# Performance work log

Hardware: AMD Instinct MI355X
Metric: run time of the kernel (lower is better)

## Reference

```python
import jax, jax.numpy as jnp
import numpy as np

B, S, D, V, T, NS, NG = 16, 512, 400, 32000, 8, 30, 3


def setup_inputs() -> dict:
    key = jax.random.key(0)
    ks = jax.random.split(key, 14)
    w = 1.0 / np.sqrt(D)
    return {
        "encoded_hidden": jax.random.normal(ks[0], (1, B, D), jnp.float32) * 0.1,
        "encoded_outputs": jax.random.normal(ks[1], (B, S, D), jnp.float32) * 0.1,
        "story": jax.random.randint(ks[2], (B, S), 0, V),
        "trg_batches": jax.random.randint(ks[3], (B, NS, T), 0, V),
        "shared_emb": jax.random.normal(ks[4], (V, D), jnp.float32) * 0.1,
        "slot_emb": jax.random.normal(ks[5], (1, D), jnp.float32) * 0.1,
        "w_ih": jax.random.normal(ks[6], (3 * D, D), jnp.float32) * w,
        "w_hh": jax.random.normal(ks[7], (3 * D, D), jnp.float32) * w,
        "b_ih": jax.random.normal(ks[8], (3 * D,), jnp.float32) * w,
        "b_hh": jax.random.normal(ks[9], (3 * D,), jnp.float32) * w,
        "w_ratio_w": jax.random.normal(ks[10], (1, 3 * D), jnp.float32) * w,
        "w_ratio_b": jax.random.normal(ks[11], (1,), jnp.float32) * w,
        "w_gate_w": jax.random.normal(ks[12], (NG, D), jnp.float32) * w,
        "w_gate_b": jax.random.normal(ks[13], (NG,), jnp.float32) * w,
        "batch_size": B,
        "max_resp_len": T,
    }


def reference(encoded_hidden, encoded_outputs, story, trg_batches, shared_emb,
              slot_emb, w_ih, w_hh, b_ih, b_hh, w_ratio_w, w_ratio_b,
              w_gate_w, w_gate_b, batch_size, max_resp_len):
    # Original torch code returns inside the slot loop -> only slot 0 is decoded.
    # h0 is re-used as GRU initial state at EVERY step (no carried hidden), and
    # teacher forcing makes each step's input known, so all T steps vectorize.
    h0 = encoded_hidden[0]                         # (B, D)
    Bq, Tq = batch_size, max_resp_len
    Vq = shared_emb.shape[0]

    # decoder inputs: step 0 = slot embedding, steps 1..T-1 = emb(trg[:,0,i-1])
    x0 = jnp.broadcast_to(slot_emb, h0.shape)      # (B, D)
    xt = shared_emb[trg_batches[:, 0, : Tq - 1]]   # (B, T-1, D)
    X = jnp.concatenate([x0[:, None, :], xt], axis=1)  # (B, T, D)

    # GRU cell (torch gate order r, z, n), h0 broadcast over steps
    gi = X @ w_ih.T + b_ih                         # (B, T, 3D)
    gh = h0 @ w_hh.T + b_hh                        # (B, 3D)
    i_r, i_z, i_n = jnp.split(gi, 3, axis=-1)
    h_r, h_z, h_n = jnp.split(gh, 3, axis=-1)
    r = jax.nn.sigmoid(i_r + h_r[:, None, :])
    z = jax.nn.sigmoid(i_z + h_z[:, None, :])
    n = jnp.tanh(i_n + r * h_n[:, None, :])
    h = (1.0 - z) * n + z * h0[:, None, :]         # (B, T, D) decoder_state == hidden

    # attention over history (no length masking: all lens == S)
    scores = jnp.einsum('btd,bsd->bts', h, encoded_outputs)   # (B, T, S)
    probs = jax.nn.softmax(scores, axis=-1)
    # FAITHFUL to original bug: context uses raw scores, not probs
    context = jnp.einsum('bts,bsd->btd', scores, encoded_outputs)

    gate0 = context[:, 0, :] @ w_gate_w.T + w_gate_b          # (B, NG), step i==0

    p_vocab = jax.nn.softmax(h @ shared_emb.T, axis=-1)       # (B, T, V)
    p_gen = jax.nn.sigmoid(
        jnp.concatenate([h, context, X], axis=-1) @ w_ratio_w.T + w_ratio_b
    )                                                         # (B, T, 1)

    # pointer distribution: scatter_add probs onto vocab ids of the story
    p_ctx = jnp.zeros((Bq, Tq, Vq), p_vocab.dtype).at[
        jnp.arange(Bq)[:, None, None],
        jnp.arange(Tq)[None, :, None],
        story[:, None, :],
    ].add(probs)

    p_final = p_gen * p_vocab + (1.0 - p_gen) * p_ctx         # (B, T, V)

    ptr_outputs = jnp.zeros((NS, Bq, Tq, Vq), p_final.dtype).at[0].set(p_final)
    gate_outputs = jnp.zeros((NS, Bq, NG), gate0.dtype).at[0].set(gate0)
    return ptr_outputs, gate_outputs
```

## Files before the change

kernel.cpp:

```cpp
#include <hip/hip_runtime.h>

#define Bq 16
#define Sq 512
#define Dq 400
#define Vq 32000
#define Tq 8
#define NSq 30
#define NGq 3
#define BTq (Bq*Tq)
#define SLICE 4096000
#define PTR_TOTAL (30ull*SLICE)
#define GATE_TOTAL (NSq*Bq*NGq)

#define ZTOT 29696000ull
#define ZPER 16384
#define GZB 256
#define AZB 384
#define LZB 1173

#define NCOMPUTE 250
#define GCOMPUTE 64

#define FBLK 8
#define FCH (Vq/FBLK)

__device__ inline float sigmoidf_(float x) { return 1.0f / (1.0f + __expf(-x)); }

__device__ inline unsigned bf16rne(float x) {
    unsigned u = __float_as_uint(x);
    return (u + 0x7FFFu + ((u >> 16) & 1u)) >> 16;
}

__device__ inline float blockReduceSum(float v, float* red) {
    int tid = threadIdx.x;
    #pragma unroll
    for (int o = 32; o > 0; o >>= 1) v += __shfl_down(v, o, 64);
    if ((tid & 63) == 0) red[tid >> 6] = v;
    __syncthreads();
    if (tid == 0) {
        float s = red[0];
        int nw = blockDim.x >> 6;
        for (int i = 1; i < nw; i++) s += red[i];
        red[0] = s;
    }
    __syncthreads();
    float r = red[0];
    __syncthreads();
    return r;
}

__device__ inline float blockReduceMax(float v, float* red) {
    int tid = threadIdx.x;
    #pragma unroll
    for (int o = 32; o > 0; o >>= 1) v = fmaxf(v, __shfl_down(v, o, 64));
    if ((tid & 63) == 0) red[tid >> 6] = v;
    __syncthreads();
    if (tid == 0) {
        float s = red[0];
        int nw = blockDim.x >> 6;
        for (int i = 1; i < nw; i++) s = fmaxf(s, red[i]);
        red[0] = s;
    }
    __syncthreads();
    float r = red[0];
    __syncthreads();
    return r;
}

__global__ __launch_bounds__(256) void k_gates(const float* __restrict__ enc_hidden,
                                               const float* __restrict__ shared_emb,
                                               const float* __restrict__ slot_emb,
                                               const float* __restrict__ w_ih,
                                               const float* __restrict__ w_hh,
                                               const float* __restrict__ b_ih,
                                               const float* __restrict__ b_hh,
                                               const int* __restrict__ trg,
                                               float* __restrict__ gi, float* __restrict__ gh,
                                               float* __restrict__ out) {
    int tid = threadIdx.x;
    if (blockIdx.x >= GCOMPUTE) {
        int zb = blockIdx.x - GCOMPUTE;
        float4 z = make_float4(0.0f, 0.0f, 0.0f, 0.0f);
        float4* dst = (float4*)(out + (size_t)SLICE);
        size_t base = (size_t)zb * ZPER + tid;
        #pragma unroll
        for (int r = 0; r < ZPER / 256; ++r) {
            size_t idx = base + (size_t)r * 256;
            if (idx < ZTOT) dst[idx] = z;
        }
        return;
    }
    __shared__ float A[9][Dq];
    __shared__ int toks[8];
    int b = blockIdx.x >> 2, jt = blockIdx.x & 3;
    if (tid < 7) toks[tid + 1] = trg[b * (NSq * Tq) + tid];
    __syncthreads();
    for (int idx = tid; idx < 900; idx += 256) {
        int r = idx / 100, q = idx - r * 100;
        const float4* src;
        if (r == 8)      src = (const float4*)(enc_hidden + b * Dq);
        else if (r == 0) src = (const float4*)slot_emb;
        else             src = (const float4*)(shared_emb + (size_t)toks[r] * Dq);
        *(float4*)&A[r][4 * q] = src[q];
    }
    __syncthreads();
    for (int o = tid; o < 2700; o += 256) {
        int r = o / 300, jj = o - r * 300;
        int j = jt * 300 + jj;
        const float* w = (r == 8) ? w_hh : w_ih;
        const float4* w4 = (const float4*)(w + (size_t)j * Dq);
        const float4* a4 = (const float4*)&A[r][0];
        float acc = (r == 8) ? b_hh[j] : b_ih[j];
        #pragma unroll 4
        for (int q = 0; q < Dq / 4; ++q) {
            float4 wv = w4[q], av = a4[q];
            acc += av.x * wv.x + av.y * wv.y + av.z * wv.z + av.w * wv.w;
        }
        if (r == 8) gh[b * 1200 + j] = acc;
        else        gi[(b * 8 + r) * 1200 + j] = acc;
    }
}

__global__ __launch_bounds__(512) void k_attn(const float* __restrict__ gi,
                                              const float* __restrict__ gh,
                                              const float* __restrict__ enc_hidden,
                                              const float* __restrict__ shared_emb,
                                              const float* __restrict__ slot_emb,
                                              const int* __restrict__ trg,
                                              const float* __restrict__ enc_out,
                                              const int* __restrict__ story,
                                              const float* __restrict__ w_ratio_w,
                                              const float* __restrict__ w_ratio_b,
                                              const float* __restrict__ w_gate_w,
                                              const float* __restrict__ w_gate_b,
                                              float* __restrict__ probs, float* __restrict__ pgen,
                                              float* __restrict__ hT, float* __restrict__ out_gate,
                                              float* __restrict__ out) {
    int tid = threadIdx.x;
    if (blockIdx.x >= BTq) {
        int zb = GZB + (blockIdx.x - BTq);
        float4 z = make_float4(0.0f, 0.0f, 0.0f, 0.0f);
        float4* dst = (float4*)(out + (size_t)SLICE);
        size_t base = (size_t)zb * ZPER + tid;
        #pragma unroll
        for (int r = 0; r < ZPER / 512; ++r) {
            size_t idx = base + (size_t)r * 512;
            if (idx < ZTOT) dst[idx] = z;
        }
        return;
    }
    __shared__ float h_l[Dq], ctx_l[Dq], x_l[Dq], sc_l[Sq], red[8];
    int bt = blockIdx.x, b = bt >> 3, t = bt & 7;
    if (tid < Dq) {
        int d = tid;
        float x = (t == 0) ? slot_emb[d]
                           : shared_emb[(size_t)trg[b * (NSq * Tq) + (t - 1)] * Dq + d];
        float h0 = enc_hidden[b * Dq + d];
        const float* gib = gi + bt * 1200;
        const float* ghb = gh + b * 1200;
        float r_ = sigmoidf_(gib[d] + ghb[d]);
        float z  = sigmoidf_(gib[Dq + d] + ghb[Dq + d]);
        float n  = tanhf(gib[2 * Dq + d] + r_ * ghb[2 * Dq + d]);
        float h  = (1.0f - z) * n + z * h0;
        h_l[d] = h; x_l[d] = x;
        hT[d * BTq + bt] = h;
    }
    __syncthreads();
    {
        const float4* e4 = (const float4*)(enc_out + ((size_t)(b * Sq + tid)) * Dq);
        float acc = 0.0f;
        for (int q = 0; q < Dq / 4; ++q) {
            float4 p = e4[q];
            int k = 4 * q;
            acc += h_l[k]*p.x + h_l[k+1]*p.y + h_l[k+2]*p.z + h_l[k+3]*p.w;
        }
        sc_l[tid] = acc;
    }
    __syncthreads();
    float myv = sc_l[tid];
    float m = blockReduceMax(myv, red);
    float e = __expf(myv - m);
    float ssum = blockReduceSum(e, red);
    probs[bt * Sq + tid] = e / ssum;
    for (int d = tid; d < Dq; d += 512) {
        float acc = 0.0f;
        #pragma unroll 8
        for (int s = 0; s < Sq; ++s)
            acc += sc_l[s] * enc_out[((size_t)(b * Sq + s)) * Dq + d];
        ctx_l[d] = acc;
    }
    __syncthreads();
    {
        float part = 0.0f;
        for (int i = tid; i < 1200; i += 512) {
            float v = (i < Dq) ? h_l[i] : (i < 2 * Dq ? ctx_l[i - Dq] : x_l[i - 2 * Dq]);
            part += v * w_ratio_w[i];
        }
        float tot = blockReduceSum(part, red);
        if (tid == 0) pgen[bt] = sigmoidf_(tot + w_ratio_b[0]);
    }
    if (t == 0) {
        for (int g = 0; g < NGq; ++g) {
            float part = 0.0f;
            for (int d = tid; d < Dq; d += 512) part += ctx_l[d] * w_gate_w[g * Dq + d];
            float tot = blockReduceSum(part, red);
            if (tid == 0) out_gate[b * NGq + g] = tot + w_gate_b[g];
        }
    }
}

#define TVL 128
#define CKL 40
__global__ __launch_bounds__(256) void k_logits(const float* __restrict__ hT,
                                                const float* __restrict__ emb,
                                                unsigned short* __restrict__ logits,
                                                float* __restrict__ pmax,
                                                float* __restrict__ psum,
                                                float* __restrict__ out) {
    __shared__ float eT[CKL][132];
    __shared__ float hL[CKL][132];
    int bid = blockIdx.x;
    int tid = threadIdx.x;
    if (bid >= NCOMPUTE) {
        int zl = bid - NCOMPUTE;
        float4 z = make_float4(0.0f, 0.0f, 0.0f, 0.0f);
        if (zl < LZB) {
            int zb = GZB + AZB + zl;
            float4* dst = (float4*)(out + (size_t)SLICE);
            size_t base = (size_t)zb * ZPER + tid;
            #pragma unroll
            for (int r = 0; r < ZPER / 256; ++r) {
                size_t idx = base + (size_t)r * 256;
                if (idx < ZTOT) dst[idx] = z;
            }
        } else {
            float4* g = (float4*)(out + PTR_TOTAL + Bq * NGq);
            for (int i = tid; i < (GATE_TOTAL - Bq * NGq) / 4; i += 256) g[i] = z;
        }
        return;
    }
    int v0 = bid * TVL;
    int tx = tid & 15, ty = tid >> 4;
    float acc[8][8];
    #pragma unroll
    for (int j = 0; j < 8; ++j)
        #pragma unroll
        for (int i = 0; i < 8; ++i) acc[j][i] = 0.0f;

    for (int c = 0; c < Dq / CKL; ++c) {
        int k0 = c * CKL;
        const float4* hg = (const float4*)(hT + (size_t)k0 * BTq);
        #pragma unroll
        for (int r = 0; r < 5; ++r) {
            int idx = tid + 256 * r;
            int k = idx >> 5, c4 = idx & 31;
            float4 vd = hg[idx];
            *(float4*)&hL[k][4 * c4] = vd;
        }
        #pragma unroll
        for (int r = 0; r < 5; ++r) {
            int idx = tid + 256 * r;
            int v = idx / 10, q = idx - 10 * v;
            float4 vd = *(const float4*)(emb + (size_t)(v0 + v) * Dq + k0 + 4 * q);
            eT[4*q+0][v] = vd.x; eT[4*q+1][v] = vd.y; eT[4*q+2][v] = vd.z; eT[4*q+3][v] = vd.w;
        }
        __syncthreads();
        #pragma unroll 4
        for (int k = 0; k < CKL; ++k) {
            float4 h0 = *(const float4*)&hL[k][8 * ty];
            float4 h1 = *(const float4*)&hL[k][8 * ty + 4];
            float4 e0 = *(const float4*)&eT[k][8 * tx];
            float4 e1 = *(const float4*)&eT[k][8 * tx + 4];
            float hv[8] = {h0.x, h0.y, h0.z, h0.w, h1.x, h1.y, h1.z, h1.w};
            float ev[8] = {e0.x, e0.y, e0.z, e0.w, e1.x, e1.y, e1.z, e1.w};
            #pragma unroll
            for (int j = 0; j < 8; ++j)
                #pragma unroll
                for (int i = 0; i < 8; ++i)
                    acc[j][i] += hv[j] * ev[i];
        }
        __syncthreads();
    }
    #pragma unroll
    for (int j = 0; j < 8; ++j) {
        int bt = 8 * ty + j;
        unsigned bb[8];
        float r[8];
        float m = -1e30f;
        #pragma unroll
        for (int i = 0; i < 8; ++i) {
            bb[i] = bf16rne(acc[j][i]);
            r[i] = __uint_as_float(bb[i] << 16);
            m = fmaxf(m, r[i]);
        }
        #pragma unroll
        for (int o = 8; o >= 1; o >>= 1) m = fmaxf(m, __shfl_xor(m, o, 16));
        float es = 0.0f;
        #pragma unroll
        for (int i = 0; i < 8; ++i) es += __expf(r[i] - m);
        #pragma unroll
        for (int o = 8; o >= 1; o >>= 1) es += __shfl_xor(es, o, 16);
        if (tx == 0) {
            pmax[bid * BTq + bt] = m;
            psum[bid * BTq + bt] = es;
        }
        uint4 w = make_uint4(bb[0] | (bb[1] << 16), bb[2] | (bb[3] << 16),
                             bb[4] | (bb[5] << 16), bb[6] | (bb[7] << 16));
        *(uint4*)(logits + (size_t)bt * Vq + v0 + 8 * tx) = w;
    }
}

__global__ __launch_bounds__(256) void k_final(const unsigned short* __restrict__ logits,
                                               const float* __restrict__ probs,
                                               const int* __restrict__ story,
                                               const float* __restrict__ pgen,
                                               const float* __restrict__ pmax,
                                               const float* __restrict__ psum,
                                               float* __restrict__ out) {
    __shared__ float chunk[FCH];
    __shared__ float red[4];
    int bid = blockIdx.x, tid = threadIdx.x;
    int bt = bid >> 3, ch = bid & 7, b = bt >> 3;
    float pm = (tid < NCOMPUTE) ? pmax[tid * BTq + bt] : -1e30f;
    float m = blockReduceMax(pm, red);
    float part = (tid < NCOMPUTE) ? psum[tid * BTq + bt] * __expf(pm - m) : 0.0f;
    float s = blockReduceSum(part, red);
    float inv = 1.0f / s, pg = pgen[bt], cg = 1.0f - pg;
    int lo = ch * FCH;
    const uint4* l4 = (const uint4*)(logits + (size_t)bt * Vq + lo);
    for (int i = tid; i < FCH / 8; i += 256) {
        uint4 lv = l4[i];
        float f0 = __uint_as_float(lv.x << 16), f1 = __uint_as_float(lv.x & 0xFFFF0000u);
        float f2 = __uint_as_float(lv.y << 16), f3 = __uint_as_float(lv.y & 0xFFFF0000u);
        float f4 = __uint_as_float(lv.z << 16), f5 = __uint_as_float(lv.z & 0xFFFF0000u);
        float f6 = __uint_as_float(lv.w << 16), f7 = __uint_as_float(lv.w & 0xFFFF0000u);
        chunk[8 * i + 0] = pg * __expf(f0 - m) * inv;
        chunk[8 * i + 1] = pg * __expf(f1 - m) * inv;
        chunk[8 * i + 2] = pg * __expf(f2 - m) * inv;
        chunk[8 * i + 3] = pg * __expf(f3 - m) * inv;
        chunk[8 * i + 4] = pg * __expf(f4 - m) * inv;
        chunk[8 * i + 5] = pg * __expf(f5 - m) * inv;
        chunk[8 * i + 6] = pg * __expf(f6 - m) * inv;
        chunk[8 * i + 7] = pg * __expf(f7 - m) * inv;
    }
    __syncthreads();
    for (int ss = tid; ss < Sq; ss += 256) {
        int rel = story[b * Sq + ss] - lo;
        if (rel >= 0 && rel < FCH)
            atomicAdd(&chunk[rel], cg * probs[bt * Sq + ss]);
    }
    __syncthreads();
    float4* o4 = (float4*)(out + (size_t)bt * Vq + lo);
    const float4* c4 = (const float4*)chunk;
    for (int i = tid; i < FCH / 4; i += 256) o4[i] = c4[i];
}

extern "C" void kernel_launch(void* const* d_in, const int* in_sizes, int n_in,
                              void* d_out, int out_size, void* d_ws, size_t ws_size,
                              hipStream_t stream) {
    const float* enc_hidden = (const float*)d_in[0];
    const float* enc_out    = (const float*)d_in[1];
    const int*   story      = (const int*)d_in[2];
    const int*   trg        = (const int*)d_in[3];
    const float* shared_emb = (const float*)d_in[4];
    const float* slot_emb   = (const float*)d_in[5];
    const float* w_ih       = (const float*)d_in[6];
    const float* w_hh       = (const float*)d_in[7];
    const float* b_ih       = (const float*)d_in[8];
    const float* b_hh       = (const float*)d_in[9];
    const float* w_ratio_w  = (const float*)d_in[10];
    const float* w_ratio_b  = (const float*)d_in[11];
    const float* w_gate_w   = (const float*)d_in[12];
    const float* w_gate_b   = (const float*)d_in[13];

    float* out = (float*)d_out;

    float* ws = (float*)d_ws;
    unsigned short* logits_buf = (unsigned short*)ws;
    float* probs_buf  = ws + (size_t)SLICE;
    float* gi_buf     = ws + 2 * (size_t)SLICE;
    float* gh_buf     = gi_buf + 153600;
    float* hT_buf     = gh_buf + 19200;
    float* pgen_buf   = hT_buf + 51200;
    float* pmax_buf   = pgen_buf + 128;
    float* psum_buf   = pmax_buf + 32000;

    hipLaunchKernelGGL(k_gates, dim3(GCOMPUTE + GZB), dim3(256), 0, stream,
                       enc_hidden, shared_emb, slot_emb, w_ih, w_hh, b_ih, b_hh, trg,
                       gi_buf, gh_buf, out);
    hipLaunchKernelGGL(k_attn, dim3(BTq + AZB), dim3(512), 0, stream,
                       gi_buf, gh_buf, enc_hidden, shared_emb, slot_emb, trg,
                       enc_out, story, w_ratio_w, w_ratio_b, w_gate_w, w_gate_b,
                       probs_buf, pgen_buf, hT_buf, out + PTR_TOTAL, out);
    hipLaunchKernelGGL(k_logits, dim3(NCOMPUTE + LZB + 1), dim3(256), 0, stream,
                       hT_buf, shared_emb, logits_buf, pmax_buf, psum_buf, out);
    hipLaunchKernelGGL(k_final, dim3(BTq * FBLK), dim3(256), 0, stream,
                       logits_buf, probs_buf, story, pgen_buf, pmax_buf, psum_buf, out);
}
```

Baseline: 742.6 us.

## Fuse GRU gate matvecs into attention kernel and use nontemporal zero stores

Removes the separate k_gates launch and computes the GRU input and hidden gate projections inside each k_attn block, keeping the results in shared memory instead of a global workspace. Its zero-fill blocks are folded into k_attn and k_logits by retuning the block counts. The large zero-fill and final output writes now use nontemporal stores to avoid polluting the cache. In exchange, each of the 128 attention blocks recomputes the hidden-state projection redundantly and streams the full w_ih and w_hh matrices, adding per-block latency before attention starts.

```diff
diff --git a/kernel.cpp b/kernel.cpp
--- a/kernel.cpp
+++ b/kernel.cpp
@@ -14,15 +14,15 @@
 
 #define ZTOT 29696000ull
 #define ZPER 16384
-#define GZB 256
-#define AZB 384
+#define AZB 640
 #define LZB 1173
 
 #define NCOMPUTE 250
-#define GCOMPUTE 64
 
 #define FBLK 8
 #define FCH (Vq/FBLK)
+
+typedef float f4nt __attribute__((ext_vector_type(4)));
 
 __device__ inline float sigmoidf_(float x) { return 1.0f / (1.0f + __expf(-x)); }
 
@@ -67,65 +67,13 @@
     return r;
 }
 
-__global__ __launch_bounds__(256) void k_gates(const float* __restrict__ enc_hidden,
-                                               const float* __restrict__ shared_emb,
-                                               const float* __restrict__ slot_emb,
-                                               const float* __restrict__ w_ih,
-                                               const float* __restrict__ w_hh,
-                                               const float* __restrict__ b_ih,
-                                               const float* __restrict__ b_hh,
-                                               const int* __restrict__ trg,
-                                               float* __restrict__ gi, float* __restrict__ gh,
-                                               float* __restrict__ out) {
-    int tid = threadIdx.x;
-    if (blockIdx.x >= GCOMPUTE) {
-        int zb = blockIdx.x - GCOMPUTE;
-        float4 z = make_float4(0.0f, 0.0f, 0.0f, 0.0f);
-        float4* dst = (float4*)(out + (size_t)SLICE);
-        size_t base = (size_t)zb * ZPER + tid;
-        #pragma unroll
-        for (int r = 0; r < ZPER / 256; ++r) {
-            size_t idx = base + (size_t)r * 256;
-            if (idx < ZTOT) dst[idx] = z;
-        }
-        return;
-    }
-    __shared__ float A[9][Dq];
-    __shared__ int toks[8];
-    int b = blockIdx.x >> 2, jt = blockIdx.x & 3;
-    if (tid < 7) toks[tid + 1] = trg[b * (NSq * Tq) + tid];
-    __syncthreads();
-    for (int idx = tid; idx < 900; idx += 256) {
-        int r = idx / 100, q = idx - r * 100;
-        const float4* src;
-        if (r == 8)      src = (const float4*)(enc_hidden + b * Dq);
-        else if (r == 0) src = (const float4*)slot_emb;
-        else             src = (const float4*)(shared_emb + (size_t)toks[r] * Dq);
-        *(float4*)&A[r][4 * q] = src[q];
-    }
-    __syncthreads();
-    for (int o = tid; o < 2700; o += 256) {
-        int r = o / 300, jj = o - r * 300;
-        int j = jt * 300 + jj;
-        const float* w = (r == 8) ? w_hh : w_ih;
-        const float4* w4 = (const float4*)(w + (size_t)j * Dq);
-        const float4* a4 = (const float4*)&A[r][0];
-        float acc = (r == 8) ? b_hh[j] : b_ih[j];
-        #pragma unroll 4
-        for (int q = 0; q < Dq / 4; ++q) {
-            float4 wv = w4[q], av = a4[q];
-            acc += av.x * wv.x + av.y * wv.y + av.z * wv.z + av.w * wv.w;
-        }
-        if (r == 8) gh[b * 1200 + j] = acc;
-        else        gi[(b * 8 + r) * 1200 + j] = acc;
-    }
-}
-
-__global__ __launch_bounds__(512) void k_attn(const float* __restrict__ gi,
-                                              const float* __restrict__ gh,
-                                              const float* __restrict__ enc_hidden,
+__global__ __launch_bounds__(512) void k_attn(const float* __restrict__ enc_hidden,
                                               const float* __restrict__ shared_emb,
                                               const float* __restrict__ slot_emb,
+                                              const float* __restrict__ w_ih,
+                                              const float* __restrict__ w_hh,
+                                              const float* __restrict__ b_ih,
+                                              const float* __restrict__ b_hh,
                                               const int* __restrict__ trg,
                                               const float* __restrict__ enc_out,
                                               const int* __restrict__ story,
@@ -138,31 +86,53 @@
                                               float* __restrict__ out) {
     int tid = threadIdx.x;
     if (blockIdx.x >= BTq) {
-        int zb = GZB + (blockIdx.x - BTq);
-        float4 z = make_float4(0.0f, 0.0f, 0.0f, 0.0f);
-        float4* dst = (float4*)(out + (size_t)SLICE);
+        int zb = blockIdx.x - BTq;
+        f4nt z = (f4nt)(0.0f);
+        f4nt* dst = (f4nt*)(out + (size_t)SLICE);
         size_t base = (size_t)zb * ZPER + tid;
         #pragma unroll
         for (int r = 0; r < ZPER / 512; ++r) {
             size_t idx = base + (size_t)r * 512;
-            if (idx < ZTOT) dst[idx] = z;
+            if (idx < ZTOT) __builtin_nontemporal_store(z, &dst[idx]);
         }
         return;
     }
-    __shared__ float h_l[Dq], ctx_l[Dq], x_l[Dq], sc_l[Sq], red[8];
+    __shared__ float x_l[Dq], h0_l[Dq], h_l[Dq], ctx_l[Dq], sc_l[Sq];
+    __shared__ float gi_l[1200], gh_l[1200];
+    __shared__ float red[8];
     int bt = blockIdx.x, b = bt >> 3, t = bt & 7;
+    if (tid < 100) {
+        const float4* src = (t == 0) ? (const float4*)slot_emb
+            : (const float4*)(shared_emb + (size_t)trg[b * (NSq * Tq) + (t - 1)] * Dq);
+        *(float4*)&x_l[4 * tid] = src[tid];
+    } else if (tid >= 256 && tid < 356) {
+        int q = tid - 256;
+        *(float4*)&h0_l[4 * q] = ((const float4*)(enc_hidden + b * Dq))[q];
+    }
+    __syncthreads();
+    for (int j = tid; j < 1200; j += 512) {
+        const float4* wi4 = (const float4*)(w_ih + (size_t)j * Dq);
+        const float4* wh4 = (const float4*)(w_hh + (size_t)j * Dq);
+        const float4* x4  = (const float4*)x_l;
+        const float4* h4  = (const float4*)h0_l;
+        float ai = b_ih[j], ah = b_hh[j];
+        #pragma unroll 4
+        for (int q = 0; q < Dq / 4; ++q) {
+            float4 wv = wi4[q], av = x4[q];
+            ai += av.x * wv.x + av.y * wv.y + av.z * wv.z + av.w * wv.w;
+            float4 wh = wh4[q], hv = h4[q];
+            ah += hv.x * wh.x + hv.y * wh.y + hv.z * wh.z + hv.w * wh.w;
+        }
+        gi_l[j] = ai; gh_l[j] = ah;
+    }
+    __syncthreads();
     if (tid < Dq) {
         int d = tid;
-        float x = (t == 0) ? slot_emb[d]
-                           : shared_emb[(size_t)trg[b * (NSq * Tq) + (t - 1)] * Dq + d];
-        float h0 = enc_hidden[b * Dq + d];
-        const float* gib = gi + bt * 1200;
-        const float* ghb = gh + b * 1200;
-        float r_ = sigmoidf_(gib[d] + ghb[d]);
-        float z  = sigmoidf_(gib[Dq + d] + ghb[Dq + d]);
-        float n  = tanhf(gib[2 * Dq + d] + r_ * ghb[2 * Dq + d]);
-        float h  = (1.0f - z) * n + z * h0;
-        h_l[d] = h; x_l[d] = x;
+        float r_ = sigmoidf_(gi_l[d] + gh_l[d]);
+        float z  = sigmoidf_(gi_l[Dq + d] + gh_l[Dq + d]);
+        float n  = tanhf(gi_l[2 * Dq + d] + r_ * gh_l[2 * Dq + d]);
+        float h  = (1.0f - z) * n + z * h0_l[d];
+        h_l[d] = h;
         hT[d * BTq + bt] = h;
     }
     __syncthreads();
@@ -223,19 +193,20 @@
     int tid = threadIdx.x;
     if (bid >= NCOMPUTE) {
         int zl = bid - NCOMPUTE;
-        float4 z = make_float4(0.0f, 0.0f, 0.0f, 0.0f);
         if (zl < LZB) {
-            int zb = GZB + AZB + zl;
-            float4* dst = (float4*)(out + (size_t)SLICE);
+            int zb = AZB + zl;
+            f4nt z = (f4nt)(0.0f);
+            f4nt* dst = (f4nt*)(out + (size_t)SLICE);
             size_t base = (size_t)zb * ZPER + tid;
             #pragma unroll
             for (int r = 0; r < ZPER / 256; ++r) {
                 size_t idx = base + (size_t)r * 256;
-                if (idx < ZTOT) dst[idx] = z;
+                if (idx < ZTOT) __builtin_nontemporal_store(z, &dst[idx]);
             }
         } else {
+            float4 z4 = make_float4(0.0f, 0.0f, 0.0f, 0.0f);
             float4* g = (float4*)(out + PTR_TOTAL + Bq * NGq);
-            for (int i = tid; i < (GATE_TOTAL - Bq * NGq) / 4; i += 256) g[i] = z;
+            for (int i = tid; i < (GATE_TOTAL - Bq * NGq) / 4; i += 256) g[i] = z4;
         }
         return;
     }
@@ -350,9 +321,10 @@
             atomicAdd(&chunk[rel], cg * probs[bt * Sq + ss]);
     }
     __syncthreads();
-    float4* o4 = (float4*)(out + (size_t)bt * Vq + lo);
-    const float4* c4 = (const float4*)chunk;
-    for (int i = tid; i < FCH / 4; i += 256) o4[i] = c4[i];
+    f4nt* o4 = (f4nt*)(out + (size_t)bt * Vq + lo);
+    const f4nt* c4 = (const f4nt*)chunk;
+    for (int i = tid; i < FCH / 4; i += 256)
+        __builtin_nontemporal_store(c4[i], &o4[i]);
 }
 
 extern "C" void kernel_launch(void* const* d_in, const int* in_sizes, int n_in,
@@ -378,18 +350,13 @@
     float* ws = (float*)d_ws;
     unsigned short* logits_buf = (unsigned short*)ws;
     float* probs_buf  = ws + (size_t)SLICE;
-    float* gi_buf     = ws + 2 * (size_t)SLICE;
-    float* gh_buf     = gi_buf + 153600;
-    float* hT_buf     = gh_buf + 19200;
+    float* hT_buf     = ws + 2 * (size_t)SLICE;
     float* pgen_buf   = hT_buf + 51200;
     float* pmax_buf   = pgen_buf + 128;
     float* psum_buf   = pmax_buf + 32000;
 
-    hipLaunchKernelGGL(k_gates, dim3(GCOMPUTE + GZB), dim3(256), 0, stream,
+    hipLaunchKernelGGL(k_attn, dim3(BTq + AZB), dim3(512), 0, stream,
                        enc_hidden, shared_emb, slot_emb, w_ih, w_hh, b_ih, b_hh, trg,
-                       gi_buf, gh_buf, out);
-    hipLaunchKernelGGL(k_attn, dim3(BTq + AZB), dim3(512), 0, stream,
-                       gi_buf, gh_buf, enc_hidden, shared_emb, slot_emb, trg,
                        enc_out, story, w_ratio_w, w_ratio_b, w_gate_w, w_gate_b,
                        probs_buf, pgen_buf, hT_buf, out + PTR_TOTAL, out);
     hipLaunchKernelGGL(k_logits, dim3(NCOMPUTE + LZB + 1), dim3(256), 0, stream,
```

New measurement: 735.7 us. No clear change (-0.9%).
